# Performance work log

Hardware: AMD Instinct MI355X
Metric: run time of the kernel (lower is better)

The kernel has to match this reference:

```python
import jax, jax.numpy as jnp
import numpy as np

MEM_DIM = 256
NUM_CHILDREN = 16
BATCH = 16384


def setup_inputs() -> dict:
    key = jax.random.key(0)
    k1, k2, k3, k4, k5, k6 = jax.random.split(key, 6)
    D = MEM_DIM
    s = 1.0 / np.sqrt(D)
    return {
        "children_memory": jax.random.normal(k1, (NUM_CHILDREN, BATCH, D), jnp.float32),
        "children_hidden": jax.random.normal(k2, (NUM_CHILDREN, BATCH, D), jnp.float32),
        "Wf": jax.random.normal(k3, (D, D), jnp.float32) * s,
        "bf": jax.random.normal(k4, (D,), jnp.float32) * s,
        "Wiou": jax.random.normal(k5, (3 * D, D), jnp.float32) * s,
        "biou": jax.random.normal(k6, (3 * D,), jnp.float32) * s,
    }


def reference(children_memory, children_hidden, Wf, bf, Wiou, biou):
    D = Wf.shape[0]
    # sum of children hidden states over the child axis -> [B, D]
    hidden_sum = jnp.sum(children_hidden, axis=0)
    # per-child forget gates: [C, B, D]
    forget_gates = jax.nn.sigmoid(jnp.einsum("cbd,ed->cbe", children_hidden, Wf) + bf)
    # i/o/u gates from summed hidden: [B, 3D]
    iou = jnp.einsum("bd,ed->be", hidden_sum, Wiou) + biou
    input_gate = jax.nn.sigmoid(iou[:, :D])
    output_gate = jax.nn.sigmoid(iou[:, D:2 * D])
    memory_gate = jnp.tanh(iou[:, 2 * D:])
    node_memory = input_gate * memory_gate + jnp.sum(forget_gates * children_memory, axis=0)
    node_hidden = output_gate * jnp.tanh(node_memory)
    return node_memory, node_hidden
```

## Files before the change

### kernel.cpp

```cpp
#include <hip/hip_runtime.h>
#include <hip/hip_bf16.h>

#define CC 16
#define BB 16384
#define DD 256
#define BT 16
#define NT 512
#define SLAB ((size_t)BB * DD)

typedef float f32x4 __attribute__((ext_vector_type(4)));
typedef short bf16x8 __attribute__((ext_vector_type(8)));
typedef short bf16x4 __attribute__((ext_vector_type(4)));

static __device__ __forceinline__ short bfc(float f) {
    return (short)__builtin_bit_cast(unsigned short, __float2bfloat16(f));
}
static __device__ __forceinline__ bf16x8 pack8(f32x4 a, f32x4 b) {
    bf16x8 v;
    v[0] = bfc(a[0]); v[1] = bfc(a[1]); v[2] = bfc(a[2]); v[3] = bfc(a[3]);
    v[4] = bfc(b[0]); v[5] = bfc(b[1]); v[6] = bfc(b[2]); v[7] = bfc(b[3]);
    return v;
}
static __device__ __forceinline__ float sigm(float x) {
    return __builtin_amdgcn_rcpf(1.0f + __expf(-x));
}
static __device__ __forceinline__ float tanh_(float x) {
    return 2.0f * __builtin_amdgcn_rcpf(1.0f + __expf(-2.0f * x)) - 1.0f;
}

__global__ void prep(const float* __restrict__ Wf, const float* __restrict__ Wiou,
                     short* __restrict__ ws) {
    const int row = blockIdx.x;
    const int t   = threadIdx.x;
    const float* src = (row < 256) ? (Wf + (size_t)row * DD)
                                   : (Wiou + (size_t)(row - 256) * DD);
    f32x4 v = *(const f32x4*)(src + t * 4);
    bf16x4 o; o[0] = bfc(v[0]); o[1] = bfc(v[1]); o[2] = bfc(v[2]); o[3] = bfc(v[3]);
    *(bf16x4*)(ws + (size_t)row * DD + t * 4) = o;
}

__global__ __launch_bounds__(NT, 3) void treelstm(
    const float* __restrict__ cmem,
    const float* __restrict__ chid,
    const short* __restrict__ wpk,
    const float* __restrict__ bfv,
    const float* __restrict__ biou,
    float* __restrict__ out)
{
    __shared__ __align__(64) unsigned char hb[2][BT * DD * 2];

    const int tid  = threadIdx.x;
    const int lane = tid & 63;
    const int wid  = tid >> 6;
    const int l15  = lane & 15;
    const int l4   = lane >> 4;
    const int b0   = blockIdx.x * BT;
    const int wc0  = wid * 32;
    const int sw15 = (l15 & 7) << 4;

    const int srow = tid >> 5;
    const int scol = (tid & 31) * 8;
    const float* hg = chid + (size_t)(b0 + srow) * DD + scol;
    const int wb = srow * 512 + ((scol * 2) ^ ((srow & 7) << 4));

    f32x4 q0 = *(const f32x4*)(hg);
    f32x4 q1 = *(const f32x4*)(hg + 4);

    bf16x8 wfr[2][8];
    float bfr[2];
#pragma unroll
    for (int n = 0; n < 2; ++n) {
        const short* wr = wpk + (size_t)(wc0 + n * 16 + l15) * DD + l4 * 8;
#pragma unroll
        for (int k = 0; k < 8; ++k) wfr[n][k] = *(const bf16x8*)(wr + k * 32);
        bfr[n] = bfv[wc0 + n * 16 + l15];
    }

    float hs[8], nmv[8];
#pragma unroll
    for (int i = 0; i < 8; ++i) { hs[i] = 0.f; nmv[i] = 0.f; }

    const float* cmp = cmem + (size_t)(b0 + l4 * 4) * DD + wc0 + l15;
    float cmA[8], cmB[8];
    f32x4 p0, p1;

    {
        const float* h1 = hg + SLAB;
        p0 = *(const f32x4*)(h1);
        p1 = *(const f32x4*)(h1 + 4);
#pragma unroll
        for (int n = 0; n < 2; ++n)
#pragma unroll
            for (int j = 0; j < 4; ++j) cmA[n * 4 + j] = cmp[j * DD + n * 16];
#pragma unroll
        for (int i = 0; i < 4; ++i) { hs[i] += q0[i]; hs[4 + i] += q1[i]; }
        *(bf16x8*)(&hb[0][0] + wb) = pack8(q0, q1);
        q0 = p0; q1 = p1;
        asm volatile("s_waitcnt lgkmcnt(0)" ::: "memory");
        __builtin_amdgcn_s_barrier();
        __builtin_amdgcn_sched_barrier(0);
    }

#define CHILD(c, PAR, Q0, Q1, P0, P1, CMU, CMF)                               \
    {                                                                         \
        if ((c) + 2 < CC) {                                                   \
            const float* hn = hg + (size_t)((c) + 2) * SLAB;                  \
            P0 = *(const f32x4*)(hn);                                         \
            P1 = *(const f32x4*)(hn + 4);                                     \
        }                                                                     \
        if ((c) + 1 < CC) {                                                   \
            const float* cn = cmp + (size_t)((c) + 1) * SLAB;                 \
            _Pragma("unroll") for (int n = 0; n < 2; ++n)                     \
            _Pragma("unroll") for (int j = 0; j < 4; ++j)                     \
                CMF[n * 4 + j] = cn[j * DD + n * 16];                         \
        }                                                                     \
        f32x4 acc0 = {bfr[0], bfr[0], bfr[0], bfr[0]};                        \
        f32x4 acc1 = {bfr[1], bfr[1], bfr[1], bfr[1]};                        \
        const unsigned char* bc = &hb[PAR][0] + l15 * 512;                    \
        _Pragma("unroll") for (int kk = 0; kk < 8; ++kk) {                    \
            bf16x8 a = *(const bf16x8*)(bc + (((kk << 6) + (l4 << 4)) ^ sw15)); \
            acc0 = __builtin_amdgcn_mfma_f32_16x16x32_bf16(a, wfr[0][kk], acc0, 0, 0, 0); \
            acc1 = __builtin_amdgcn_mfma_f32_16x16x32_bf16(a, wfr[1][kk], acc1, 0, 0, 0); \
        }                                                                     \
        _Pragma("unroll") for (int j = 0; j < 4; ++j) {                       \
            nmv[j]     += sigm(acc0[j]) * CMU[j];                             \
            nmv[4 + j] += sigm(acc1[j]) * CMU[4 + j];                         \
        }                                                                     \
        if ((c) + 1 < CC) {                                                   \
            _Pragma("unroll") for (int i = 0; i < 4; ++i) {                   \
                hs[i] += Q0[i]; hs[4 + i] += Q1[i];                           \
            }                                                                 \
            *(bf16x8*)(&hb[(PAR) ^ 1][0] + wb) = pack8(Q0, Q1);               \
            asm volatile("s_waitcnt lgkmcnt(0)" ::: "memory");                \
            __builtin_amdgcn_s_barrier();                                     \
            __builtin_amdgcn_sched_barrier(0);                                \
        }                                                                     \
    }

    for (int cc = 0; cc < CC; cc += 2) {
        CHILD(cc,     0, q0, q1, p0, p1, cmA, cmB);
        CHILD(cc + 1, 1, p0, p1, q0, q1, cmB, cmA);
    }
#undef CHILD

    {
        f32x4 e0 = {hs[0], hs[1], hs[2], hs[3]};
        f32x4 e1 = {hs[4], hs[5], hs[6], hs[7]};
        *(bf16x8*)(&hb[0][0] + wb) = pack8(e0, e1);
    }
    asm volatile("s_waitcnt lgkmcnt(0)" ::: "memory");
    __builtin_amdgcn_s_barrier();
    __builtin_amdgcn_sched_barrier(0);

    bf16x8 afr[8];
    {
        const unsigned char* bc = &hb[0][0] + l15 * 512;
#pragma unroll
        for (int kk = 0; kk < 8; ++kk)
            afr[kk] = *(const bf16x8*)(bc + (((kk << 6) + (l4 << 4)) ^ sw15));
    }

    float gq[3][8];
#pragma unroll
    for (int q = 0; q < 3; ++q) {
#pragma unroll
        for (int n = 0; n < 2; ++n) {
            const short* wr = wpk + (size_t)(256 + q * 256 + wc0 + n * 16 + l15) * DD + l4 * 8;
            f32x4 acc = {0.f, 0.f, 0.f, 0.f};
#pragma unroll
            for (int kk = 0; kk < 8; ++kk)
                acc = __builtin_amdgcn_mfma_f32_16x16x32_bf16(afr[kk], *(const bf16x8*)(wr + kk * 32), acc, 0, 0, 0);
            float bq = biou[q * 256 + wc0 + n * 16 + l15];
#pragma unroll
            for (int j = 0; j < 4; ++j) gq[q][n * 4 + j] = acc[j] + bq;
        }
    }

    float* o0 = out + (size_t)(b0 + l4 * 4) * DD + wc0 + l15;
    float* o1 = o0 + SLAB;
#pragma unroll
    for (int n = 0; n < 2; ++n)
#pragma unroll
        for (int j = 0; j < 4; ++j) {
            float ig = sigm(gq[0][n * 4 + j]);
            float og = sigm(gq[1][n * 4 + j]);
            float ug = tanh_(gq[2][n * 4 + j]);
            float mm = nmv[n * 4 + j] + ig * ug;
            float hh = og * tanh_(mm);
            o0[j * DD + n * 16] = mm;
            o1[j * DD + n * 16] = hh;
        }
}

extern "C" void kernel_launch(void* const* d_in, const int* in_sizes, int n_in,
                              void* d_out, int out_size, void* d_ws, size_t ws_size,
                              hipStream_t stream) {
    const float* cmem = (const float*)d_in[0];
    const float* chid = (const float*)d_in[1];
    const float* Wf   = (const float*)d_in[2];
    const float* bf   = (const float*)d_in[3];
    const float* Wiou = (const float*)d_in[4];
    const float* biou = (const float*)d_in[5];
    float* out = (float*)d_out;
    short* wpk = (short*)d_ws;

    prep<<<1024, 64, 0, stream>>>(Wf, Wiou, wpk);
    treelstm<<<BB / BT, NT, 0, stream>>>(cmem, chid, wpk, bf, biou, out);
}
```

Measured before the change: 162.8 us.

## Process two children per barrier with split-K MFMA chains and full-XOR LDS swizzle

The child loop now stages two children's hidden tiles per LDS buffer and swaps buffers once per pair, so the number of block barriers is halved. Each child's forget-gate GEMM splits K across two independent accumulator chains to shorten MFMA dependency latency. The LDS swizzle now XORs the full 32-chunk index with the row, and the occupancy hint rises from 3 to 4 blocks per CU. The cost is more registers held across iterations and doubled LDS per block, which could cap occupancy or cause spills.

```diff
diff --git a/kernel.cpp b/kernel.cpp
--- a/kernel.cpp
+++ b/kernel.cpp
@@ -39,7 +39,7 @@
     *(bf16x4*)(ws + (size_t)row * DD + t * 4) = o;
 }
 
-__global__ __launch_bounds__(NT, 3) void treelstm(
+__global__ __launch_bounds__(NT, 4) void treelstm(
     const float* __restrict__ cmem,
     const float* __restrict__ chid,
     const short* __restrict__ wpk,
@@ -47,7 +47,7 @@
     const float* __restrict__ biou,
     float* __restrict__ out)
 {
-    __shared__ __align__(64) unsigned char hb[2][BT * DD * 2];
+    __shared__ __align__(64) unsigned char hb[2][2][BT * DD * 2];
 
     const int tid  = threadIdx.x;
     const int lane = tid & 63;
@@ -56,15 +56,17 @@
     const int l4   = lane >> 4;
     const int b0   = blockIdx.x * BT;
     const int wc0  = wid * 32;
-    const int sw15 = (l15 & 7) << 4;
-
-    const int srow = tid >> 5;
-    const int scol = (tid & 31) * 8;
-    const float* hg = chid + (size_t)(b0 + srow) * DD + scol;
-    const int wb = srow * 512 + ((scol * 2) ^ ((srow & 7) << 4));
-
-    f32x4 q0 = *(const f32x4*)(hg);
-    f32x4 q1 = *(const f32x4*)(hg + 4);
+    const int swr  = l15 << 4;
+
+    const int srow   = tid >> 5;
+    const int schunk = tid & 31;
+    const float* hg  = chid + (size_t)(b0 + srow) * DD + schunk * 8;
+    const int wb     = srow * 512 + (((schunk ^ srow) & 31) << 4);
+
+    f32x4 hA0 = *(const f32x4*)(hg);
+    f32x4 hA1 = *(const f32x4*)(hg + 4);
+    f32x4 hA2 = *(const f32x4*)(hg + SLAB);
+    f32x4 hA3 = *(const f32x4*)(hg + SLAB + 4);
 
     bf16x8 wfr[2][8];
     float bfr[2];
@@ -76,88 +78,127 @@
         bfr[n] = bfv[wc0 + n * 16 + l15];
     }
 
+    const float* cmp = cmem + (size_t)(b0 + l4 * 4) * DD + wc0 + l15;
+    float cmE[8], cmO[8];
+#pragma unroll
+    for (int n = 0; n < 2; ++n)
+#pragma unroll
+        for (int j = 0; j < 4; ++j) cmE[n * 4 + j] = cmp[j * DD + n * 16];
+
     float hs[8], nmv[8];
 #pragma unroll
     for (int i = 0; i < 8; ++i) { hs[i] = 0.f; nmv[i] = 0.f; }
 
-    const float* cmp = cmem + (size_t)(b0 + l4 * 4) * DD + wc0 + l15;
-    float cmA[8], cmB[8];
-    f32x4 p0, p1;
-
-    {
-        const float* h1 = hg + SLAB;
-        p0 = *(const f32x4*)(h1);
-        p1 = *(const f32x4*)(h1 + 4);
-#pragma unroll
-        for (int n = 0; n < 2; ++n)
-#pragma unroll
-            for (int j = 0; j < 4; ++j) cmA[n * 4 + j] = cmp[j * DD + n * 16];
-#pragma unroll
-        for (int i = 0; i < 4; ++i) { hs[i] += q0[i]; hs[4 + i] += q1[i]; }
-        *(bf16x8*)(&hb[0][0] + wb) = pack8(q0, q1);
-        q0 = p0; q1 = p1;
-        asm volatile("s_waitcnt lgkmcnt(0)" ::: "memory");
-        __builtin_amdgcn_s_barrier();
-        __builtin_amdgcn_sched_barrier(0);
-    }
-
-#define CHILD(c, PAR, Q0, Q1, P0, P1, CMU, CMF)                               \
-    {                                                                         \
-        if ((c) + 2 < CC) {                                                   \
-            const float* hn = hg + (size_t)((c) + 2) * SLAB;                  \
-            P0 = *(const f32x4*)(hn);                                         \
-            P1 = *(const f32x4*)(hn + 4);                                     \
-        }                                                                     \
-        if ((c) + 1 < CC) {                                                   \
-            const float* cn = cmp + (size_t)((c) + 1) * SLAB;                 \
-            _Pragma("unroll") for (int n = 0; n < 2; ++n)                     \
-            _Pragma("unroll") for (int j = 0; j < 4; ++j)                     \
-                CMF[n * 4 + j] = cn[j * DD + n * 16];                         \
-        }                                                                     \
-        f32x4 acc0 = {bfr[0], bfr[0], bfr[0], bfr[0]};                        \
-        f32x4 acc1 = {bfr[1], bfr[1], bfr[1], bfr[1]};                        \
-        const unsigned char* bc = &hb[PAR][0] + l15 * 512;                    \
-        _Pragma("unroll") for (int kk = 0; kk < 8; ++kk) {                    \
-            bf16x8 a = *(const bf16x8*)(bc + (((kk << 6) + (l4 << 4)) ^ sw15)); \
-            acc0 = __builtin_amdgcn_mfma_f32_16x16x32_bf16(a, wfr[0][kk], acc0, 0, 0, 0); \
-            acc1 = __builtin_amdgcn_mfma_f32_16x16x32_bf16(a, wfr[1][kk], acc1, 0, 0, 0); \
-        }                                                                     \
-        _Pragma("unroll") for (int j = 0; j < 4; ++j) {                       \
-            nmv[j]     += sigm(acc0[j]) * CMU[j];                             \
-            nmv[4 + j] += sigm(acc1[j]) * CMU[4 + j];                         \
-        }                                                                     \
-        if ((c) + 1 < CC) {                                                   \
-            _Pragma("unroll") for (int i = 0; i < 4; ++i) {                   \
-                hs[i] += Q0[i]; hs[4 + i] += Q1[i];                           \
-            }                                                                 \
-            *(bf16x8*)(&hb[(PAR) ^ 1][0] + wb) = pack8(Q0, Q1);               \
-            asm volatile("s_waitcnt lgkmcnt(0)" ::: "memory");                \
-            __builtin_amdgcn_s_barrier();                                     \
-            __builtin_amdgcn_sched_barrier(0);                                \
-        }                                                                     \
-    }
-
-    for (int cc = 0; cc < CC; cc += 2) {
-        CHILD(cc,     0, q0, q1, p0, p1, cmA, cmB);
-        CHILD(cc + 1, 1, p0, p1, q0, q1, cmB, cmA);
-    }
-#undef CHILD
-
-    {
-        f32x4 e0 = {hs[0], hs[1], hs[2], hs[3]};
-        f32x4 e1 = {hs[4], hs[5], hs[6], hs[7]};
-        *(bf16x8*)(&hb[0][0] + wb) = pack8(e0, e1);
-    }
+#pragma unroll
+    for (int i = 0; i < 4; ++i) {
+        hs[i] += hA0[i] + hA2[i];
+        hs[4 + i] += hA1[i] + hA3[i];
+    }
+    *(bf16x8*)(&hb[0][0][0] + wb) = pack8(hA0, hA1);
+    *(bf16x8*)(&hb[0][1][0] + wb) = pack8(hA2, hA3);
     asm volatile("s_waitcnt lgkmcnt(0)" ::: "memory");
     __builtin_amdgcn_s_barrier();
     __builtin_amdgcn_sched_barrier(0);
 
+    const float* hgn = hg + 2 * SLAB;
+    const float* cmn = cmp + SLAB;
+
+#pragma unroll 1
+    for (int P = 0; P < 8; ++P) {
+        if (P < 7) {
+            hA0 = *(const f32x4*)(hgn);
+            hA1 = *(const f32x4*)(hgn + 4);
+            hA2 = *(const f32x4*)(hgn + SLAB);
+            hA3 = *(const f32x4*)(hgn + SLAB + 4);
+            hgn += 2 * SLAB;
+        }
+#pragma unroll
+        for (int n = 0; n < 2; ++n)
+#pragma unroll
+            for (int j = 0; j < 4; ++j) cmO[n * 4 + j] = cmn[j * DD + n * 16];
+        cmn += SLAB;
+
+        f32x4 e0 = {bfr[0], bfr[0], bfr[0], bfr[0]};
+        f32x4 e1 = {bfr[1], bfr[1], bfr[1], bfr[1]};
+        f32x4 e2 = {0.f, 0.f, 0.f, 0.f}, e3 = {0.f, 0.f, 0.f, 0.f};
+        const unsigned char* bcE = &hb[P & 1][0][0] + l15 * 512;
+#pragma unroll
+        for (int kk = 0; kk < 4; ++kk) {
+            bf16x8 a = *(const bf16x8*)(bcE + ((((kk) << 6) + (l4 << 4)) ^ swr));
+            e0 = __builtin_amdgcn_mfma_f32_16x16x32_bf16(a, wfr[0][kk], e0, 0, 0, 0);
+            e1 = __builtin_amdgcn_mfma_f32_16x16x32_bf16(a, wfr[1][kk], e1, 0, 0, 0);
+        }
+#pragma unroll
+        for (int kk = 4; kk < 8; ++kk) {
+            bf16x8 a = *(const bf16x8*)(bcE + ((((kk) << 6) + (l4 << 4)) ^ swr));
+            e2 = __builtin_amdgcn_mfma_f32_16x16x32_bf16(a, wfr[0][kk], e2, 0, 0, 0);
+            e3 = __builtin_amdgcn_mfma_f32_16x16x32_bf16(a, wfr[1][kk], e3, 0, 0, 0);
+        }
+#pragma unroll
+        for (int j = 0; j < 4; ++j) {
+            nmv[j]     += sigm(e0[j] + e2[j]) * cmE[j];
+            nmv[4 + j] += sigm(e1[j] + e3[j]) * cmE[4 + j];
+        }
+        if (P < 7) {
+#pragma unroll
+            for (int n = 0; n < 2; ++n)
+#pragma unroll
+                for (int j = 0; j < 4; ++j) cmE[n * 4 + j] = cmn[j * DD + n * 16];
+        }
+        cmn += SLAB;
+
+        f32x4 o0 = {bfr[0], bfr[0], bfr[0], bfr[0]};
+        f32x4 o1 = {bfr[1], bfr[1], bfr[1], bfr[1]};
+        f32x4 o2 = {0.f, 0.f, 0.f, 0.f}, o3 = {0.f, 0.f, 0.f, 0.f};
+        const unsigned char* bcO = &hb[P & 1][1][0] + l15 * 512;
+#pragma unroll
+        for (int kk = 0; kk < 4; ++kk) {
+            bf16x8 a = *(const bf16x8*)(bcO + ((((kk) << 6) + (l4 << 4)) ^ swr));
+            o0 = __builtin_amdgcn_mfma_f32_16x16x32_bf16(a, wfr[0][kk], o0, 0, 0, 0);
+            o1 = __builtin_amdgcn_mfma_f32_16x16x32_bf16(a, wfr[1][kk], o1, 0, 0, 0);
+        }
+#pragma unroll
+        for (int kk = 4; kk < 8; ++kk) {
+            bf16x8 a = *(const bf16x8*)(bcO + ((((kk) << 6) + (l4 << 4)) ^ swr));
+            o2 = __builtin_amdgcn_mfma_f32_16x16x32_bf16(a, wfr[0][kk], o2, 0, 0, 0);
+            o3 = __builtin_amdgcn_mfma_f32_16x16x32_bf16(a, wfr[1][kk], o3, 0, 0, 0);
+        }
+
+        if (P < 7) {
+#pragma unroll
+            for (int i = 0; i < 4; ++i) {
+                hs[i] += hA0[i] + hA2[i];
+                hs[4 + i] += hA1[i] + hA3[i];
+            }
+            *(bf16x8*)(&hb[(P & 1) ^ 1][0][0] + wb) = pack8(hA0, hA1);
+            *(bf16x8*)(&hb[(P & 1) ^ 1][1][0] + wb) = pack8(hA2, hA3);
+            asm volatile("s_waitcnt lgkmcnt(0)" ::: "memory");
+            __builtin_amdgcn_s_barrier();
+            __builtin_amdgcn_sched_barrier(0);
+        }
+
+#pragma unroll
+        for (int j = 0; j < 4; ++j) {
+            nmv[j]     += sigm(o0[j] + o2[j]) * cmO[j];
+            nmv[4 + j] += sigm(o1[j] + o3[j]) * cmO[4 + j];
+        }
+    }
+
+    {
+        f32x4 s0 = {hs[0], hs[1], hs[2], hs[3]};
+        f32x4 s1 = {hs[4], hs[5], hs[6], hs[7]};
+        *(bf16x8*)(&hb[0][0][0] + wb) = pack8(s0, s1);
+    }
+    asm volatile("s_waitcnt lgkmcnt(0)" ::: "memory");
+    __builtin_amdgcn_s_barrier();
+    __builtin_amdgcn_sched_barrier(0);
+
     bf16x8 afr[8];
     {
-        const unsigned char* bc = &hb[0][0] + l15 * 512;
+        const unsigned char* bc = &hb[0][0][0] + l15 * 512;
 #pragma unroll
         for (int kk = 0; kk < 8; ++kk)
-            afr[kk] = *(const bf16x8*)(bc + (((kk << 6) + (l4 << 4)) ^ sw15));
+            afr[kk] = *(const bf16x8*)(bc + (((kk << 6) + (l4 << 4)) ^ swr));
     }
 
     float gq[3][8];
@@ -176,8 +217,8 @@
         }
     }
 
-    float* o0 = out + (size_t)(b0 + l4 * 4) * DD + wc0 + l15;
-    float* o1 = o0 + SLAB;
+    float* o0p = out + (size_t)(b0 + l4 * 4) * DD + wc0 + l15;
+    float* o1p = o0p + SLAB;
 #pragma unroll
     for (int n = 0; n < 2; ++n)
 #pragma unroll
@@ -187,8 +228,8 @@
             float ug = tanh_(gq[2][n * 4 + j]);
             float mm = nmv[n * 4 + j] + ig * ug;
             float hh = og * tanh_(mm);
-            o0[j * DD + n * 16] = mm;
-            o1[j * DD + n * 16] = hh;
+            o0p[j * DD + n * 16] = mm;
+            o1p[j * DD + n * 16] = hh;
         }
 }
 
```

After: 442.3 us. 172% more time.
